# Kernel optimization log

Hardware: AMD Instinct MI355X
Metric: run time of the kernel (lower is better)

The kernel has to match this reference:

```python
import jax, jax.numpy as jnp
import numpy as np

NUM_HEADS = 12

def setup_inputs() -> dict:
    key = jax.random.key(0)
    k1, k2, k3 = jax.random.split(key, 3)
    B, N, D = 16, 1024, 768
    x = jax.random.normal(k1, (B, N, D), dtype=jnp.float32)
    w_qkv = jax.random.normal(k2, (D, 3 * D), dtype=jnp.float32) * (D ** -0.5)
    b_qkv = jnp.zeros((3 * D,), dtype=jnp.float32)
    w_proj = jax.random.normal(k3, (D, D), dtype=jnp.float32) * (D ** -0.5)
    b_proj = jnp.zeros((D,), dtype=jnp.float32)
    return {"x": x, "w_qkv": w_qkv, "b_qkv": b_qkv, "w_proj": w_proj, "b_proj": b_proj}

def reference(x, w_qkv, b_qkv, w_proj, b_proj):
    B, N, D = x.shape
    H = NUM_HEADS
    Hd = D // H
    scale = Hd ** -0.5
    qkv = x @ w_qkv + b_qkv                       # (B, N, 3D)
    qkv = qkv.reshape(B, N, 3, H, Hd)
    q, k, v = qkv[:, :, 0], qkv[:, :, 1], qkv[:, :, 2]  # (B, N, H, Hd)
    attn = jnp.einsum('bnhd,bmhd->bhnm', q, k) * scale  # (B, H, N, N)
    attn = jax.nn.softmax(attn, axis=-1)
    out = jnp.einsum('bhnm,bmhd->bnhd', attn, v).reshape(B, N, D)
    return out @ w_proj + b_proj
```

## Files before the change

### kernel.cpp

```cpp
#include <hip/hip_runtime.h>


typedef _Float16 half8 __attribute__((ext_vector_type(8)));
typedef _Float16 half4 __attribute__((ext_vector_type(4)));
typedef __fp16   fp16x2 __attribute__((ext_vector_type(2)));
typedef float    f32x4  __attribute__((ext_vector_type(4)));
typedef float    f32x16 __attribute__((ext_vector_type(16)));
typedef unsigned int u32x4 __attribute__((ext_vector_type(4)));

#define DI __device__ __forceinline__

constexpr int   BATCH  = 16;
constexpr int   SEQ    = 1024;
constexpr int   DM     = 768;
constexpr int   NH     = 12;
constexpr int   HD     = 64;
constexpr float SCALE  = 0.125f;
constexpr float LOG2E  = 1.4426950408889634f;

DI void async16(const _Float16* g, _Float16* l) {
  __builtin_amdgcn_global_load_lds(
      (const __attribute__((address_space(1))) void*)g,
      (__attribute__((address_space(3))) void*)l, 16, 0, 0);
}

DI void copy16(_Float16* dst, const _Float16* src) {
  *(u32x4*)dst = *(const u32x4*)src;
}

DI int pack_rtz(float a, float b) {
  union { fp16x2 h; int i; } u;
  u.h = __builtin_amdgcn_cvt_pkrtz(a, b);
  return u.i;
}

__global__ void cvt_x_kernel(const float* __restrict__ x,
                             _Float16* __restrict__ xh, int n4) {
  int i = blockIdx.x * 256 + threadIdx.x;
  if (i >= n4) return;
  float4 v = ((const float4*)x)[i];
  half4 h;
  h[0] = (_Float16)v.x; h[1] = (_Float16)v.y;
  h[2] = (_Float16)v.z; h[3] = (_Float16)v.w;
  *(half4*)(xh + (size_t)i * 4) = h;
}

__global__ void cvt_wt2_kernel(const float* __restrict__ wq,
                               _Float16* __restrict__ wqT,
                               const float* __restrict__ wp,
                               _Float16* __restrict__ wpT) {
  __shared__ float tile[32][33];
  const int by = blockIdx.y;
  const float* w; _Float16* wt; int N, nb;
  if (by < 72) { w = wq; wt = wqT; N = 2304; nb = by * 32; }
  else         { w = wp; wt = wpT; N = 768;  nb = (by - 72) * 32; }
  const int K = 768;
  int kb = blockIdx.x * 32;
  int tx = threadIdx.x & 31, ty = threadIdx.x >> 5;
#pragma unroll
  for (int i = 0; i < 32; i += 8)
    tile[ty + i][tx] = w[(size_t)(kb + ty + i) * N + nb + tx];
  __syncthreads();
#pragma unroll
  for (int i = 0; i < 32; i += 8)
    wt[(size_t)(nb + ty + i) * K + kb + tx] = (_Float16)tile[tx][ty + i];
}

__launch_bounds__(256, 4)
__global__ void gemm_qkv_kernel(const _Float16* __restrict__ A,
                                const _Float16* __restrict__ Bt,
                                const float* __restrict__ bias,
                                _Float16* __restrict__ Qo,
                                _Float16* __restrict__ Ko,
                                _Float16* __restrict__ VTo) {
  __shared__ _Float16 As[128 * 32];
  __shared__ _Float16 Bs[128 * 32];
  __shared__ _Float16 Cs[64 * 136];
  const int tid  = threadIdx.x;
  const int lin  = blockIdx.x;
  const int xcd  = lin & 7, j = lin >> 3;
  const int ct   = j % 18;
  const int m0   = ((j / 18) * 8 + xcd) * 128;
  const int n0   = ct * 128;
  const int w    = tid >> 6, lane = tid & 63;
  const int quad = lane >> 4, l15 = lane & 15;
  const int wr   = w >> 1, wc = w & 1;

  f32x4 acc[4][4] = {};

  const int e  = tid * 8;
  const int rA = e >> 5;
  const int kA = e & 31;
  const _Float16* ga = A  + (size_t)(m0 + rA) * 768 + kA;
  const _Float16* gb = Bt + (size_t)(n0 + rA) * 768 + kA;

  for (int kt = 0; kt < 24; ++kt) {
    __syncthreads();
    const int k0 = kt * 32;
    async16(ga + k0,            &As[e]);
    async16(ga + k0 + 64 * 768, &As[e + 2048]);
    async16(gb + k0,            &Bs[e]);
    async16(gb + k0 + 64 * 768, &Bs[e + 2048]);
    __syncthreads();

    half8 af[4], bf[4];
#pragma unroll
    for (int mi = 0; mi < 4; mi++)
      af[mi] = *(const half8*)&As[(wr * 64 + mi * 16 + l15) * 32 + quad * 8];
#pragma unroll
    for (int ni = 0; ni < 4; ni++)
      bf[ni] = *(const half8*)&Bs[(wc * 64 + ni * 16 + l15) * 32 + quad * 8];
#pragma unroll
    for (int mi = 0; mi < 4; mi++)
#pragma unroll
      for (int ni = 0; ni < 4; ni++)
        acc[mi][ni] = __builtin_amdgcn_mfma_f32_16x16x32_f16(
            af[mi], bf[ni], acc[mi][ni], 0, 0, 0);
  }

  const float oscale = (ct < 6) ? SCALE : 1.0f;
  float bcol[4];
#pragma unroll
  for (int ni = 0; ni < 4; ni++)
    bcol[ni] = bias[n0 + wc * 64 + ni * 16 + l15];

  const int b     = m0 >> 10;
  const int nrow0 = m0 & 1023;
  const int sec   = ct / 6;
  const int h0    = (ct % 6) * 2;

#pragma unroll
  for (int p = 0; p < 2; ++p) {
    if (p) __syncthreads();
    if (wr == p) {
#pragma unroll
      for (int mi = 0; mi < 4; mi++)
#pragma unroll
        for (int ni = 0; ni < 4; ni++) {
          int col = wc * 64 + ni * 16 + l15;
          int row = mi * 16 + quad * 4;
#pragma unroll
          for (int r = 0; r < 4; r++)
            Cs[(row + r) * 136 + col] =
                (_Float16)((acc[mi][ni][r] + bcol[ni]) * oscale);
        }
    }
    __syncthreads();

    if (sec < 2) {
      _Float16* dst = (sec == 0) ? Qo : Ko;
      int row = tid >> 2, seg = tid & 3;
      int hl = seg >> 1, off32 = (seg & 1) * 32;
      _Float16* g = dst +
          ((size_t)((b * NH + h0 + hl) * SEQ + nrow0 + p * 64 + row)) * HD + off32;
      const _Float16* s = &Cs[row * 136 + hl * 64 + off32];
      copy16(g, s);
      copy16(g + 8, s + 8);
      copy16(g + 16, s + 16);
      copy16(g + 24, s + 24);
    } else {
      int c = tid & 127, half = tid >> 7;
      int hl = c >> 6, d = c & 63;
      _Float16 tmp[32];
#pragma unroll
      for (int jj = 0; jj < 32; jj++) tmp[jj] = Cs[(half * 32 + jj) * 136 + c];
      _Float16* g = VTo + ((size_t)((b * NH + h0 + hl) * HD + d)) * SEQ
                        + nrow0 + p * 64 + half * 32;
#pragma unroll
      for (int jj = 0; jj < 4; jj++)
        copy16(g + jj * 8, (const _Float16*)&tmp[jj * 8]);
    }
  }
}

__launch_bounds__(256, 2)
__global__ void attn_kernel(const _Float16* __restrict__ Q,
                            const _Float16* __restrict__ K,
                            const _Float16* __restrict__ VT,
                            _Float16* __restrict__ Oh) {
  __shared__ _Float16 smem[2][2][64 * 72];
  _Float16* OLds = &smem[0][0][0];

  const int tid = threadIdx.x;
  const int i   = blockIdx.x;
  const int bh  = (i & 7) * 24 + ((i >> 3) >> 2);
  const int q0  = ((i >> 3) & 3) * 256;
  const int b   = bh / NH, hh = bh - b * NH;
  const int w   = tid >> 6, lane = tid & 63;
  const int l31 = lane & 31, h = lane >> 5;

  const _Float16* Qg = Q  + (size_t)bh * SEQ * HD;
  const _Float16* Kg = K  + (size_t)bh * SEQ * HD;
  const _Float16* Vg = VT + (size_t)bh * HD * SEQ;

  half8 qb[2][4];
#pragma unroll
  for (int N = 0; N < 2; N++) {
    const _Float16* qrow = Qg + (size_t)(q0 + w * 64 + N * 32 + l31) * HD + h * 8;
#pragma unroll
    for (int s = 0; s < 4; s++)
      qb[N][s] = *(const half8*)(qrow + s * 16);
  }

  const int  sr  = (tid & 127) >> 1;
  const int  sp  = tid & 1;
  const bool isK = tid < 128;
  const _Float16* sg = isK ? (Kg + sr * HD + sp * 32)
                           : (Vg + (size_t)sr * SEQ + sp * 32);
  const int sstep = isK ? 64 * HD : 64;
  const int soff  = (isK ? 0 : 64 * 72) + sr * 72 + sp * 32;

  u32x4 pf[4];
#pragma unroll
  for (int c = 0; c < 4; c++) pf[c] = *(const u32x4*)(sg + c * 8);
#pragma unroll
  for (int c = 0; c < 4; c++) *(u32x4*)(&smem[0][0][0] + soff + c * 8) = pf[c];

  f32x16 of[2][2];
#pragma unroll
  for (int D = 0; D < 2; D++)
#pragma unroll
    for (int N = 0; N < 2; N++)
#pragma unroll
      for (int r = 0; r < 16; r++) of[D][N][r] = 0.f;
  float m_[2] = {-1e30f, -1e30f}, l_[2] = {0.f, 0.f};

  for (int kt = 0; kt < 16; ++kt) {
    if (kt < 15) {
      const _Float16* nsg = sg + (kt + 1) * sstep;
#pragma unroll
      for (int c = 0; c < 4; c++) pf[c] = *(const u32x4*)(nsg + c * 8);
    }
    __syncthreads();
    const _Float16* Ks = &smem[kt & 1][0][0];
    const _Float16* Vs = &smem[kt & 1][1][0];

    f32x16 sf[2][2];
#pragma unroll
    for (int M = 0; M < 2; M++)
#pragma unroll
      for (int N = 0; N < 2; N++)
#pragma unroll
        for (int r = 0; r < 16; r++) sf[M][N][r] = 0.f;
#pragma unroll
    for (int s = 0; s < 4; s++) {
      half8 ka0 = *(const half8*)&Ks[l31 * 72 + s * 16 + h * 8];
      half8 ka1 = *(const half8*)&Ks[(32 + l31) * 72 + s * 16 + h * 8];
#pragma unroll
      for (int N = 0; N < 2; N++) {
        sf[0][N] = __builtin_amdgcn_mfma_f32_32x32x16_f16(ka0, qb[N][s], sf[0][N], 0, 0, 0);
        sf[1][N] = __builtin_amdgcn_mfma_f32_32x32x16_f16(ka1, qb[N][s], sf[1][N], 0, 0, 0);
      }
    }

    float alpha[2], c1[2], tsum[2];
#pragma unroll
    for (int N = 0; N < 2; N++) {
      float tmax = -1e30f;
#pragma unroll
      for (int r = 0; r < 16; r++)
        tmax = fmaxf(tmax, fmaxf(sf[0][N][r], sf[1][N][r]));
      tmax = fmaxf(tmax, __shfl_xor(tmax, 32, 64));
      float mnew = fmaxf(m_[N], tmax);
      alpha[N] = __builtin_amdgcn_exp2f((m_[N] - mnew) * LOG2E);
      m_[N] = mnew;
      c1[N] = mnew * LOG2E;
      tsum[N] = 0.f;
    }

    int pdw[2][2][8];
#pragma unroll
    for (int M = 0; M < 2; M++)
#pragma unroll
      for (int N = 0; N < 2; N++) {
#pragma unroll
        for (int r = 0; r < 16; r++) {
          float p = __builtin_amdgcn_exp2f(sf[M][N][r] * LOG2E - c1[N]);
          sf[M][N][r] = p;
          tsum[N] += p;
        }
#pragma unroll
        for (int u = 0; u < 8; u++)
          pdw[M][N][u] = pack_rtz(sf[M][N][2 * u], sf[M][N][2 * u + 1]);
      }
#pragma unroll
    for (int N = 0; N < 2; N++) {
      tsum[N] += __shfl_xor(tsum[N], 32, 64);
      l_[N] = l_[N] * alpha[N] + tsum[N];
    }
#pragma unroll
    for (int D = 0; D < 2; D++)
#pragma unroll
      for (int N = 0; N < 2; N++)
#pragma unroll
        for (int r = 0; r < 16; r++) of[D][N][r] *= alpha[N];

#pragma unroll
    for (int t = 0; t < 4; ++t) {
      const int M = t >> 1, s2 = (t & 1) * 4;
      half8 va0 = *(const half8*)&Vs[l31 * 72 + t * 16 + h * 8];
      half8 va1 = *(const half8*)&Vs[(32 + l31) * 72 + t * 16 + h * 8];
#pragma unroll
      for (int N = 0; N < 2; N++) {
        int a0 = pdw[M][N][s2 + 0], a1 = pdw[M][N][s2 + 1];
        int a2 = pdw[M][N][s2 + 2], a3 = pdw[M][N][s2 + 3];
        int e0 = h ? a0 : a2, e1 = h ? a1 : a3;
        int r0 = __shfl_xor(e0, 32, 64), r1 = __shfl_xor(e1, 32, 64);
        union { u32x4 u; half8 hv; } bb;
        bb.u[0] = h ? r0 : a0; bb.u[1] = h ? r1 : a1;
        bb.u[2] = h ? a2 : r0; bb.u[3] = h ? a3 : r1;
        of[0][N] = __builtin_amdgcn_mfma_f32_32x32x16_f16(va0, bb.hv, of[0][N], 0, 0, 0);
        of[1][N] = __builtin_amdgcn_mfma_f32_32x32x16_f16(va1, bb.hv, of[1][N], 0, 0, 0);
      }
    }

    if (kt < 15) {
      _Float16* dst = &smem[(kt + 1) & 1][0][0] + soff;
#pragma unroll
      for (int c = 0; c < 4; c++) *(u32x4*)(dst + c * 8) = pf[c];
    }
  }

  __syncthreads();
  float inv[2] = {1.0f / l_[0], 1.0f / l_[1]};
  int* OW = (int*)OLds;
#pragma unroll
  for (int N = 0; N < 2; N++) {
    const int q_local = w * 64 + N * 32 + l31;
#pragma unroll
    for (int D = 0; D < 2; D++)
#pragma unroll
      for (int u = 0; u < 8; u++) {
        int v = pack_rtz(of[D][N][2 * u] * inv[N], of[D][N][2 * u + 1] * inv[N]);
        int dwi = 16 * D + 4 * (u >> 1) + (u & 1) + 2 * h;
        OW[q_local * 36 + dwi] = v;
      }
  }
  __syncthreads();
#pragma unroll
  for (int p = 0; p < 8; p++) {
    int q = p * 32 + (tid >> 3), c = tid & 7;
    *(u32x4*)(Oh + (size_t)(b * SEQ + q0 + q) * DM + hh * HD + c * 8) =
        *(const u32x4*)&OLds[q * 72 + c * 8];
  }
}

__launch_bounds__(256, 4)
__global__ void gemm_proj_kernel(const _Float16* __restrict__ A,
                                 const _Float16* __restrict__ Bt,
                                 const float* __restrict__ bias,
                                 float* __restrict__ out) {
  __shared__ _Float16 As[128 * 32];
  __shared__ _Float16 Bs[128 * 32];
  const int tid  = threadIdx.x;
  const int lin  = blockIdx.x;
  const int xcd  = lin & 7, j = lin >> 3;
  const int ct   = j % 6;
  const int m0   = ((j / 6) * 8 + xcd) * 128;
  const int n0   = ct * 128;
  const int w    = tid >> 6, lane = tid & 63;
  const int quad = lane >> 4, l15 = lane & 15;
  const int wr   = w >> 1, wc = w & 1;

  f32x4 acc[4][4] = {};

  const int e  = tid * 8;
  const int rA = e >> 5;
  const int kA = e & 31;
  const _Float16* ga = A  + (size_t)(m0 + rA) * 768 + kA;
  const _Float16* gb = Bt + (size_t)(n0 + rA) * 768 + kA;

  for (int kt = 0; kt < 24; ++kt) {
    __syncthreads();
    const int k0 = kt * 32;
    async16(ga + k0,            &As[e]);
    async16(ga + k0 + 64 * 768, &As[e + 2048]);
    async16(gb + k0,            &Bs[e]);
    async16(gb + k0 + 64 * 768, &Bs[e + 2048]);
    __syncthreads();

    half8 af[4], bf[4];
#pragma unroll
    for (int mi = 0; mi < 4; mi++)
      af[mi] = *(const half8*)&As[(wr * 64 + mi * 16 + l15) * 32 + quad * 8];
#pragma unroll
    for (int ni = 0; ni < 4; ni++)
      bf[ni] = *(const half8*)&Bs[(wc * 64 + ni * 16 + l15) * 32 + quad * 8];
#pragma unroll
    for (int mi = 0; mi < 4; mi++)
#pragma unroll
      for (int ni = 0; ni < 4; ni++)
        acc[mi][ni] = __builtin_amdgcn_mfma_f32_16x16x32_f16(
            af[mi], bf[ni], acc[mi][ni], 0, 0, 0);
  }

  float bcol[4];
#pragma unroll
  for (int ni = 0; ni < 4; ni++)
    bcol[ni] = bias[n0 + wc * 64 + ni * 16 + l15];
#pragma unroll
  for (int mi = 0; mi < 4; mi++)
#pragma unroll
    for (int ni = 0; ni < 4; ni++) {
      int col = n0 + wc * 64 + ni * 16 + l15;
      int row = m0 + wr * 64 + mi * 16 + quad * 4;
#pragma unroll
      for (int r = 0; r < 4; r++)
        out[(size_t)(row + r) * 768 + col] = acc[mi][ni][r] + bcol[ni];
    }
}

extern "C" void kernel_launch(void* const* d_in, const int* in_sizes, int n_in,
                              void* d_out, int out_size, void* d_ws, size_t ws_size,
                              hipStream_t stream) {
  const float* x      = (const float*)d_in[0];
  const float* w_qkv  = (const float*)d_in[1];
  const float* b_qkv  = (const float*)d_in[2];
  const float* w_proj = (const float*)d_in[3];
  const float* b_proj = (const float*)d_in[4];
  float* out = (float*)d_out;

  char* ws = (char*)d_ws;
  _Float16* xh     = (_Float16*)(ws);
  _Float16* wqkvT  = (_Float16*)(ws + 25165824);
  _Float16* wprojT = (_Float16*)(ws + 28704768);
  _Float16* Qp     = (_Float16*)(ws + 29884416);
  _Float16* Kp     = (_Float16*)(ws + 55050240);
  _Float16* VTp    = (_Float16*)(ws + 80216064);
  _Float16* Ohp    = (_Float16*)(ws + 105381888);

  cvt_x_kernel<<<dim3(3145728 / 256), 256, 0, stream>>>(x, xh, 3145728);
  cvt_wt2_kernel<<<dim3(24, 96), 256, 0, stream>>>(w_qkv, wqkvT, w_proj, wprojT);
  gemm_qkv_kernel<<<dim3(2304), 256, 0, stream>>>(xh, wqkvT, b_qkv, Qp, Kp, VTp);
  attn_kernel<<<dim3(768), 256, 0, stream>>>(Qp, Kp, VTp, Ohp);
  gemm_proj_kernel<<<dim3(768), 256, 0, stream>>>(Ohp, wprojT, b_proj, out);
}
```

Baseline: 310.6 us.

## Double-buffer GEMM tiles via register prefetch with padded LDS rows

Both GEMM kernels stop using direct global-to-LDS async loads with two barriers per k-step. They now prefetch the next k-tile into registers while computing on the current LDS buffer, then write it into a second LDS buffer, so each step needs one barrier. LDS rows are padded from 32 to 40 halves to cut bank conflicts on the fragment reads. This costs more LDS and registers, so the occupancy hint is lowered from 4 to 3 blocks per CU.

```diff
diff --git a/kernel.cpp b/kernel.cpp
--- a/kernel.cpp
+++ b/kernel.cpp
@@ -17,12 +17,6 @@
 constexpr int   HD     = 64;
 constexpr float SCALE  = 0.125f;
 constexpr float LOG2E  = 1.4426950408889634f;
-
-DI void async16(const _Float16* g, _Float16* l) {
-  __builtin_amdgcn_global_load_lds(
-      (const __attribute__((address_space(1))) void*)g,
-      (__attribute__((address_space(3))) void*)l, 16, 0, 0);
-}
 
 DI void copy16(_Float16* dst, const _Float16* src) {
   *(u32x4*)dst = *(const u32x4*)src;
@@ -66,16 +60,15 @@
     wt[(size_t)(nb + ty + i) * K + kb + tx] = (_Float16)tile[tx][ty + i];
 }
 
-__launch_bounds__(256, 4)
+__launch_bounds__(256, 3)
 __global__ void gemm_qkv_kernel(const _Float16* __restrict__ A,
                                 const _Float16* __restrict__ Bt,
                                 const float* __restrict__ bias,
                                 _Float16* __restrict__ Qo,
                                 _Float16* __restrict__ Ko,
                                 _Float16* __restrict__ VTo) {
-  __shared__ _Float16 As[128 * 32];
-  __shared__ _Float16 Bs[128 * 32];
-  __shared__ _Float16 Cs[64 * 136];
+  __shared__ _Float16 sh[20480];
+  _Float16* Cs = sh;
   const int tid  = threadIdx.x;
   const int lin  = blockIdx.x;
   const int xcd  = lin & 7, j = lin >> 3;
@@ -90,33 +83,55 @@
 
   const int e  = tid * 8;
   const int rA = e >> 5;
-  const int kA = e & 31;
-  const _Float16* ga = A  + (size_t)(m0 + rA) * 768 + kA;
-  const _Float16* gb = Bt + (size_t)(n0 + rA) * 768 + kA;
+  const int g8 = e & 31;
+  const _Float16* ga = A  + (size_t)(m0 + rA) * 768 + g8;
+  const _Float16* gb = Bt + (size_t)(n0 + rA) * 768 + g8;
+  const int so = rA * 40 + g8;
+
+  u32x4 pA0 = *(const u32x4*)ga;
+  u32x4 pA1 = *(const u32x4*)(ga + 64 * 768);
+  u32x4 pB0 = *(const u32x4*)gb;
+  u32x4 pB1 = *(const u32x4*)(gb + 64 * 768);
+  {
+    _Float16* As = sh; _Float16* Bs = sh + 5120;
+    *(u32x4*)(As + so) = pA0; *(u32x4*)(As + so + 64 * 40) = pA1;
+    *(u32x4*)(Bs + so) = pB0; *(u32x4*)(Bs + so + 64 * 40) = pB1;
+  }
 
   for (int kt = 0; kt < 24; ++kt) {
     __syncthreads();
-    const int k0 = kt * 32;
-    async16(ga + k0,            &As[e]);
-    async16(ga + k0 + 64 * 768, &As[e + 2048]);
-    async16(gb + k0,            &Bs[e]);
-    async16(gb + k0 + 64 * 768, &Bs[e + 2048]);
-    __syncthreads();
+    if (kt < 23) {
+      const int k0 = (kt + 1) * 32;
+      pA0 = *(const u32x4*)(ga + k0);
+      pA1 = *(const u32x4*)(ga + k0 + 64 * 768);
+      pB0 = *(const u32x4*)(gb + k0);
+      pB1 = *(const u32x4*)(gb + k0 + 64 * 768);
+    }
+    const _Float16* As = sh + (kt & 1) * 10240;
+    const _Float16* Bs = As + 5120;
 
     half8 af[4], bf[4];
 #pragma unroll
     for (int mi = 0; mi < 4; mi++)
-      af[mi] = *(const half8*)&As[(wr * 64 + mi * 16 + l15) * 32 + quad * 8];
+      af[mi] = *(const half8*)&As[(wr * 64 + mi * 16 + l15) * 40 + quad * 8];
 #pragma unroll
     for (int ni = 0; ni < 4; ni++)
-      bf[ni] = *(const half8*)&Bs[(wc * 64 + ni * 16 + l15) * 32 + quad * 8];
+      bf[ni] = *(const half8*)&Bs[(wc * 64 + ni * 16 + l15) * 40 + quad * 8];
 #pragma unroll
     for (int mi = 0; mi < 4; mi++)
 #pragma unroll
       for (int ni = 0; ni < 4; ni++)
         acc[mi][ni] = __builtin_amdgcn_mfma_f32_16x16x32_f16(
             af[mi], bf[ni], acc[mi][ni], 0, 0, 0);
-  }
+
+    if (kt < 23) {
+      _Float16* Asn = sh + ((kt + 1) & 1) * 10240;
+      _Float16* Bsn = Asn + 5120;
+      *(u32x4*)(Asn + so) = pA0; *(u32x4*)(Asn + so + 64 * 40) = pA1;
+      *(u32x4*)(Bsn + so) = pB0; *(u32x4*)(Bsn + so + 64 * 40) = pB1;
+    }
+  }
+  __syncthreads();
 
   const float oscale = (ct < 6) ? SCALE : 1.0f;
   float bcol[4];
@@ -345,13 +360,12 @@
   }
 }
 
-__launch_bounds__(256, 4)
+__launch_bounds__(256, 3)
 __global__ void gemm_proj_kernel(const _Float16* __restrict__ A,
                                  const _Float16* __restrict__ Bt,
                                  const float* __restrict__ bias,
                                  float* __restrict__ out) {
-  __shared__ _Float16 As[128 * 32];
-  __shared__ _Float16 Bs[128 * 32];
+  __shared__ _Float16 sh[20480];
   const int tid  = threadIdx.x;
   const int lin  = blockIdx.x;
   const int xcd  = lin & 7, j = lin >> 3;
@@ -366,32 +380,53 @@
 
   const int e  = tid * 8;
   const int rA = e >> 5;
-  const int kA = e & 31;
-  const _Float16* ga = A  + (size_t)(m0 + rA) * 768 + kA;
-  const _Float16* gb = Bt + (size_t)(n0 + rA) * 768 + kA;
+  const int g8 = e & 31;
+  const _Float16* ga = A  + (size_t)(m0 + rA) * 768 + g8;
+  const _Float16* gb = Bt + (size_t)(n0 + rA) * 768 + g8;
+  const int so = rA * 40 + g8;
+
+  u32x4 pA0 = *(const u32x4*)ga;
+  u32x4 pA1 = *(const u32x4*)(ga + 64 * 768);
+  u32x4 pB0 = *(const u32x4*)gb;
+  u32x4 pB1 = *(const u32x4*)(gb + 64 * 768);
+  {
+    _Float16* As = sh; _Float16* Bs = sh + 5120;
+    *(u32x4*)(As + so) = pA0; *(u32x4*)(As + so + 64 * 40) = pA1;
+    *(u32x4*)(Bs + so) = pB0; *(u32x4*)(Bs + so + 64 * 40) = pB1;
+  }
 
   for (int kt = 0; kt < 24; ++kt) {
     __syncthreads();
-    const int k0 = kt * 32;
-    async16(ga + k0,            &As[e]);
-    async16(ga + k0 + 64 * 768, &As[e + 2048]);
-    async16(gb + k0,            &Bs[e]);
-    async16(gb + k0 + 64 * 768, &Bs[e + 2048]);
-    __syncthreads();
+    if (kt < 23) {
+      const int k0 = (kt + 1) * 32;
+      pA0 = *(const u32x4*)(ga + k0);
+      pA1 = *(const u32x4*)(ga + k0 + 64 * 768);
+      pB0 = *(const u32x4*)(gb + k0);
+      pB1 = *(const u32x4*)(gb + k0 + 64 * 768);
+    }
+    const _Float16* As = sh + (kt & 1) * 10240;
+    const _Float16* Bs = As + 5120;
 
     half8 af[4], bf[4];
 #pragma unroll
     for (int mi = 0; mi < 4; mi++)
-      af[mi] = *(const half8*)&As[(wr * 64 + mi * 16 + l15) * 32 + quad * 8];
+      af[mi] = *(const half8*)&As[(wr * 64 + mi * 16 + l15) * 40 + quad * 8];
 #pragma unroll
     for (int ni = 0; ni < 4; ni++)
-      bf[ni] = *(const half8*)&Bs[(wc * 64 + ni * 16 + l15) * 32 + quad * 8];
+      bf[ni] = *(const half8*)&Bs[(wc * 64 + ni * 16 + l15) * 40 + quad * 8];
 #pragma unroll
     for (int mi = 0; mi < 4; mi++)
 #pragma unroll
       for (int ni = 0; ni < 4; ni++)
         acc[mi][ni] = __builtin_amdgcn_mfma_f32_16x16x32_f16(
             af[mi], bf[ni], acc[mi][ni], 0, 0, 0);
+
+    if (kt < 23) {
+      _Float16* Asn = sh + ((kt + 1) & 1) * 10240;
+      _Float16* Bsn = Asn + 5120;
+      *(u32x4*)(Asn + so) = pA0; *(u32x4*)(Asn + so + 64 * 40) = pA1;
+      *(u32x4*)(Bsn + so) = pB0; *(u32x4*)(Bsn + so + 64 * 40) = pB1;
+    }
   }
 
   float bcol[4];
```

Measured after the change: 306.5 us. Within noise of the previous version (-1.3%).
